# Kernel optimization log

Hardware: AMD Instinct MI355X
Metric: run time of the kernel (lower is better)

Reference implementation:

```python
import jax, jax.numpy as jnp
import numpy as np

B, S, H = 4, 1024, 2048
E = 16            # num_experts
K = 2             # num_experts_per_token
I = 1024          # per-expert intermediate_dim
N_SHARED = 2
I_SHARED = I * N_SHARED
RATIO = 0.1       # shared_expert_ratio
EPS = 1e-9


def _swiglu(x, wg, wu, wd):
    # SwiGLU, bias=False: down( silu(gate(x)) * up(x) )
    return (jax.nn.silu(x @ wg) * (x @ wu)) @ wd


def setup_inputs() -> dict:
    key = jax.random.key(0)
    ks = jax.random.split(key, 9)
    scale = 0.02
    x = jax.random.normal(ks[0], (B, S, H), dtype=jnp.float32)
    centroids = jax.random.normal(ks[1], (E, H), dtype=jnp.float32)  # nn.Parameter(randn)
    gate_bias = jnp.zeros((E,), dtype=jnp.float32)
    # shared expert SwiGLU weights (intermediate = I * n_shared_experts)
    wg_s = jax.random.normal(ks[2], (H, I_SHARED), dtype=jnp.float32) * scale
    wu_s = jax.random.normal(ks[3], (H, I_SHARED), dtype=jnp.float32) * scale
    wd_s = jax.random.normal(ks[4], (I_SHARED, H), dtype=jnp.float32) * scale
    # routed experts, stacked [E, ...]
    wg = jax.random.normal(ks[5], (E, H, I), dtype=jnp.float32) * scale
    wu = jax.random.normal(ks[6], (E, H, I), dtype=jnp.float32) * scale
    wd = jax.random.normal(ks[7], (E, I, H), dtype=jnp.float32) * scale
    return {"x": x, "centroids": centroids, "gate_bias": gate_bias,
            "wg_s": wg_s, "wu_s": wu_s, "wd_s": wd_s,
            "wg": wg, "wu": wu, "wd": wd}


def reference(x, centroids, gate_bias, wg_s, wu_s, wd_s, wg, wu, wd):
    # 1) shared expert on ALL tokens, scaled by ratio
    shared = _swiglu(x, wg_s, wu_s, wd_s) * RATIO          # [B,S,H]
    # 2) centroid affinity (DeepSeek-V3 sigmoid gating)
    affinity = jax.nn.sigmoid(jnp.einsum('bsh,eh->bse', x, centroids))  # [B,S,E]
    # 3) bias used ONLY for selection
    biased = affinity + gate_bias
    _, top_idx = jax.lax.top_k(biased, K)                  # [B,S,K]
    # 4) clean weights from unbiased affinity, normalized to sum 1
    top_aff = jnp.take_along_axis(affinity, top_idx, axis=-1)  # [B,S,K]
    weights = top_aff / (top_aff.sum(-1, keepdims=True) + EPS)
    # 5) combine-mask: per-token per-expert weight (0 if not selected)
    mask = (jax.nn.one_hot(top_idx, E, dtype=x.dtype) * weights[..., None]).sum(-2)  # [B,S,E]
    # 6) expert compute + weighted combine; loop over fixed small E avoids
    #    materializing a [B,S,E,H] tensor
    routed = jnp.zeros_like(x)
    for e in range(E):
        routed = routed + mask[..., e:e + 1] * _swiglu(x, wg[e], wu[e], wd[e])
    return shared + routed
```

## Files before the change

### kernel.cpp

```cpp
#include <hip/hip_runtime.h>
#include <hip/hip_bf16.h>

typedef unsigned short u16;
typedef unsigned int u32;
typedef unsigned long long u64;
typedef __attribute__((ext_vector_type(8))) short short8;
typedef __attribute__((ext_vector_type(4))) float f32x4;

#define TOKENS 4096
#define HDIM 2048
#define NEXP 16
#define IDIM 1024
#define ISH 2048
#define NCHUNK 128

#define GUITEMS 2304
#define DITEMS 2048

#define AS1(p) ((const __attribute__((address_space(1))) u32*)(p))
#define AS3(p) ((__attribute__((address_space(3))) u32*)(p))

__device__ __forceinline__ u16 f2b(float f) {
    u32 u = __float_as_uint(f);
    u32 r = u + 0x7fffu + ((u >> 16) & 1u);
    return (u16)(r >> 16);
}

__device__ __forceinline__ int item_index(int bid) {
    int x = bid & 7, j = bid >> 3;
    return ((x + 8 * (j >> 4)) << 4) | (j & 15);
}

__global__ __launch_bounds__(256) void route_kernel(const float* __restrict__ x,
                                                    const float* __restrict__ cent,
                                                    const float* __restrict__ bias,
                                                    u16* __restrict__ xb,
                                                    int* __restrict__ top_e,
                                                    float* __restrict__ top_w) {
    __shared__ alignas(16) float cs[8 * 2048];
    int lane = threadIdx.x & 63;
    int wv = threadIdx.x >> 6;
    int t = blockIdx.x * 4 + wv;
    const float4* xp4 = (const float4*)(x + (size_t)t * HDIM);
    float4 xr[8];
#pragma unroll
    for (int i = 0; i < 8; i++) xr[i] = xp4[lane + 64 * i];
    u16* xbp = xb + (size_t)t * HDIM;
#pragma unroll
    for (int i = 0; i < 8; i++) {
        u32 lo = (u32)f2b(xr[i].x) | ((u32)f2b(xr[i].y) << 16);
        u32 hi = (u32)f2b(xr[i].z) | ((u32)f2b(xr[i].w) << 16);
        uint2 o = make_uint2(lo, hi);
        *(uint2*)(xbp + (size_t)(lane + 64 * i) * 4) = o;
    }
    float aff[16];
#pragma unroll
    for (int ph = 0; ph < 2; ph++) {
        if (ph) __syncthreads();
        const float* sbase = cent + (size_t)(ph * 8 + wv * 2) * HDIM;
        float* dbase = cs + (size_t)wv * 2 * HDIM;
#pragma unroll
        for (int i = 0; i < 16; i++) {
            __builtin_amdgcn_global_load_lds(AS1(sbase + i * 256 + lane * 4),
                                             AS3(dbase + i * 256), 16, 0, 0);
        }
        __syncthreads();
#pragma unroll
        for (int e = 0; e < 8; e++) {
            const float4* cp = (const float4*)cs + (size_t)e * 512;
            float s = 0.f;
#pragma unroll
            for (int i = 0; i < 8; i++) {
                float4 cv = cp[lane + 64 * i];
                s += xr[i].x * cv.x;
                s += xr[i].y * cv.y;
                s += xr[i].z * cv.z;
                s += xr[i].w * cv.w;
            }
#pragma unroll
            for (int off = 32; off > 0; off >>= 1) s += __shfl_xor(s, off, 64);
            aff[ph * 8 + e] = 1.f / (1.f + expf(-s));
        }
    }
    float b0 = -1e30f, b1 = -1e30f, a0 = 0.f, a1 = 0.f;
    int e0 = -1, e1 = -1;
#pragma unroll
    for (int e = 0; e < 16; e++) {
        float v = aff[e] + bias[e];
        if (v > b0) {
            b1 = b0; e1 = e0; a1 = a0;
            b0 = v; e0 = e; a0 = aff[e];
        } else if (v > b1) {
            b1 = v; e1 = e; a1 = aff[e];
        }
    }
    float inv = 1.f / (a0 + a1 + 1e-9f);
    if (lane == 0) {
        top_e[2 * t] = e0; top_w[2 * t] = a0 * inv;
        top_e[2 * t + 1] = e1; top_w[2 * t + 1] = a1 * inv;
    }
}

__global__ __launch_bounds__(1024) void build_kernel(
    const int* __restrict__ top_e, const float* __restrict__ top_w,
    int* __restrict__ counts, int* __restrict__ offsets, int* __restrict__ itemsGU,
    int* __restrict__ itemsD, int* __restrict__ list_tok, int* __restrict__ tok2slot) {
    __shared__ int cnt[NCHUNK][16];
    __shared__ int offs_s[16];
    __shared__ int totals[16];
    __shared__ int guPref[16], dPref[16];
    int tid = threadIdx.x;
    int lane = tid & 63, wv = tid >> 6;
    for (int i = tid; i < GUITEMS; i += 1024) itemsGU[i] = -1;
    for (int i = tid; i < DITEMS; i += 1024) itemsD[i] = -1;
    for (int c = wv; c < NCHUNK; c += 16) {
        int v = top_e[c * 64 + lane];
#pragma unroll
        for (int e = 0; e < 16; e++) {
            u64 m = __ballot(v == e);
            if (lane == 0) cnt[c][e] = (int)__popcll(m);
        }
    }
    __syncthreads();
    if (tid < 16) {
        int s = 0;
        for (int c = 0; c < NCHUNK; c++) s += cnt[c][tid];
        totals[tid] = s;
        counts[tid] = s;
    }
    __syncthreads();
    if (tid == 0) {
        int r = 0, g = 0, d = 0;
        for (int e = 0; e < 16; e++) {
            offs_s[e] = r;
            offsets[e] = r;
            r += totals[e];
            guPref[e] = g;
            g += ((totals[e] + 127) >> 7) * 16;
            dPref[e] = d;
            d += ((totals[e] + 255) >> 8) * 32;
        }
    }
    {
        int i = tid;
        int g = i >> 4, s = i & 15;
        int y0 = (g >> 3) << 2, m0 = (g & 7) << 2;
        itemsGU[i] = ((m0 + (s >> 2)) << 8) | (y0 + (s & 3));
    }
    if (tid < 512) {
        int i = tid;
        int g = i >> 4, s = i & 15;
        int y0 = (g >> 2) << 2, m0 = (g & 3) << 2;
        itemsD[i] = ((m0 + (s >> 2)) << 8) | (y0 + (s & 3));
    }
    __syncthreads();
    if (tid < 16) {
        int e = tid;
        int tA = (totals[e] + 127) >> 7;
        int p = 1024 + guPref[e];
        for (int y0 = 0; y0 < 16; y0 += 4)
            for (int m = 0; m < tA; m++)
                for (int dy = 0; dy < 4; dy++)
                    itemsGU[p++] = (1 << 28) | (e << 20) | (m << 8) | (y0 + dy);
        int tB = (totals[e] + 255) >> 8;
        p = 512 + dPref[e];
        for (int y0 = 0; y0 < 32; y0 += 4)
            for (int m = 0; m < tB; m++)
                for (int dy = 0; dy < 4; dy++)
                    itemsD[p++] = (1 << 28) | (e << 20) | (m << 8) | (y0 + dy);
        int r = offs_s[e];
        for (int c = 0; c < NCHUNK; c++) {
            int v = cnt[c][e];
            cnt[c][e] = r;
            r += v;
        }
    }
    __syncthreads();
    for (int c = wv; c < NCHUNK; c += 16) {
        int i = c * 64 + lane;
        int v = top_e[i];
        int rank = 0;
#pragma unroll
        for (int e = 0; e < 16; e++) {
            u64 m = __ballot(v == e);
            if (v == e) rank = (int)__popcll(m & ((1ull << lane) - 1ull));
        }
        int slot = cnt[c][v] + rank;
        list_tok[slot] = i >> 1;
        tok2slot[i] = slot;
    }
}

__global__ __launch_bounds__(256) void conv_all_kernel(
    const float* __restrict__ wgs, const float* __restrict__ wus,
    const float* __restrict__ wds, const float* __restrict__ wg,
    const float* __restrict__ wu, const float* __restrict__ wd, u16* __restrict__ Wt_gs,
    u16* __restrict__ Wt_us, u16* __restrict__ Wt_ds, u16* __restrict__ Wt_g,
    u16* __restrict__ Wt_u, u16* __restrict__ Wt_d) {
    int id = blockIdx.x;
    const float* Wm;
    u16* Wtm;
    int K, N, nt, kc;
    if (id < 768) {
        K = 2048; N = 2048;
        int seg = id >> 8, r = id & 255;
        nt = r & 31; kc = r >> 5;
        if (seg == 0) { Wm = wgs; Wtm = Wt_gs; }
        else if (seg == 1) { Wm = wus; Wtm = Wt_us; }
        else { Wm = wds; Wtm = Wt_ds; }
    } else if (id < 4864) {
        K = 2048; N = 1024;
        int r = id - 768;
        int m = r >> 11;
        r &= 2047;
        int e = r >> 7;
        r &= 127;
        nt = r & 15; kc = r >> 4;
        size_t off = (size_t)e * 2048 * 1024;
        if (m == 0) { Wm = wg + off; Wtm = Wt_g + off; }
        else { Wm = wu + off; Wtm = Wt_u + off; }
    } else {
        K = 1024; N = 2048;
        int r = id - 4864;
        int e = r >> 7;
        r &= 127;
        nt = r & 31; kc = r >> 5;
        size_t off = (size_t)e * 1024 * 2048;
        Wm = wd + off; Wtm = Wt_d + off;
    }
    int ksB = K >> 5;
    __shared__ u16 Ls[64 * 40];
    int t = threadIdx.x;
    int kr = t >> 3, ng = t & 7;
    int nn = t >> 2, seg2 = t & 3;
    int g = seg2 ^ ((nn >> 2) & 3);
#pragma unroll
    for (int s = 0; s < 8; s++) {
        int kb = kc * 256 + s * 32;
        const float* src = Wm + (size_t)(kb + kr) * N + nt * 64 + ng * 8;
        float4 f0 = *(const float4*)src;
        float4 f1 = *(const float4*)(src + 4);
        __syncthreads();
        const float* p0 = (const float*)&f0;
        const float* p1 = (const float*)&f1;
#pragma unroll
        for (int l = 0; l < 4; l++) Ls[(8 * ng + l) * 40 + kr] = f2b(p0[l]);
#pragma unroll
        for (int l = 0; l < 4; l++) Ls[(8 * ng + 4 + l) * 40 + kr] = f2b(p1[l]);
        __syncthreads();
        const u16* lp = &Ls[nn * 40 + g * 8];
        u32 w0 = (u32)lp[0] | ((u32)lp[1] << 16);
        u32 w1 = (u32)lp[2] | ((u32)lp[3] << 16);
        u32 w2 = (u32)lp[4] | ((u32)lp[5] << 16);
        u32 w3 = (u32)lp[6] | ((u32)lp[7] << 16);
        uint4 o = make_uint4(w0, w1, w2, w3);
        *(uint4*)(Wtm + (size_t)(nt * ksB + (kb >> 5)) * 2048 + t * 8) = o;
    }
}

__global__ __launch_bounds__(256) void gemm_gateup(
    const u16* __restrict__ A, const u16* __restrict__ BgS, const u16* __restrict__ BuS,
    const u16* __restrict__ BgR, const u16* __restrict__ BuR, u16* __restrict__ hS,
    u16* __restrict__ hR, const int* __restrict__ counts, const int* __restrict__ offsets,
    const int* __restrict__ list_tok, const int* __restrict__ items) {
    int it = items[item_index(blockIdx.x)];
    if (it < 0) return;
    int routed = (it >> 28) & 1;
    int e = (it >> 20) & 15;
    int m0 = ((it >> 8) & 4095) * 128;
    int yb = it & 255;
    int cnt, base, Nout;
    const u16 *Bg, *Bu;
    u16* hout;
    if (routed) {
        cnt = counts[e];
        base = offsets[e];
        Nout = IDIM;
        size_t off = (size_t)e * HDIM * IDIM;
        Bg = BgR + off;
        Bu = BuR + off;
        hout = hR;
    } else {
        cnt = TOKENS;
        base = 0;
        Nout = ISH;
        Bg = BgS;
        Bu = BuS;
        hout = hS;
    }
    const int nk = HDIM >> 6;
    __shared__ alignas(16) u16 As[128 * 64];
    __shared__ alignas(16) u16 Bgs[64 * 64];
    __shared__ alignas(16) u16 Bus[64 * 64];
    int tid = threadIdx.x;
    int lane = tid & 63, wv = tid >> 6;
    int quad = lane >> 4, mr = lane & 15;
    int n0 = yb * 64;
    int gk = (tid & 3) ^ ((tid >> 4) & 3);
    int mg0 = min(m0 + (tid >> 2), cnt - 1);
    int mg1 = min(m0 + 64 + (tid >> 2), cnt - 1);
    size_t sr0 = routed ? (size_t)list_tok[base + mg0] : (size_t)mg0;
    size_t sr1 = routed ? (size_t)list_tok[base + mg1] : (size_t)mg1;
    const u16* ap0 = A + sr0 * HDIM + gk * 8;
    const u16* ap1 = A + sr1 * HDIM + gk * 8;
    size_t bstr = (size_t)(HDIM >> 5) * 2048;
    const u16* bgp = Bg + (size_t)yb * bstr + tid * 8;
    const u16* bup = Bu + (size_t)yb * bstr + tid * 8;
    int xq = quad ^ ((mr >> 2) & 3);
    f32x4 accg[2][4], accu[2][4];
#pragma unroll
    for (int i = 0; i < 2; i++)
#pragma unroll
        for (int j = 0; j < 4; j++) { accg[i][j] = (f32x4)0.f; accu[i][j] = (f32x4)0.f; }

    for (int ks = 0; ks < nk; ks++) {
        __syncthreads();
        __builtin_amdgcn_global_load_lds(AS1(ap0), AS3(As + wv * 512), 16, 0, 0);
        __builtin_amdgcn_global_load_lds(AS1(ap0 + 32), AS3(As + 4096 + wv * 512), 16, 0, 0);
        __builtin_amdgcn_global_load_lds(AS1(ap1), AS3(As + 2048 + wv * 512), 16, 0, 0);
        __builtin_amdgcn_global_load_lds(AS1(ap1 + 32), AS3(As + 6144 + wv * 512), 16, 0, 0);
        __builtin_amdgcn_global_load_lds(AS1(bgp), AS3(Bgs + wv * 512), 16, 0, 0);
        __builtin_amdgcn_global_load_lds(AS1(bgp + 2048), AS3(Bgs + 2048 + wv * 512), 16, 0, 0);
        __builtin_amdgcn_global_load_lds(AS1(bup), AS3(Bus + wv * 512), 16, 0, 0);
        __builtin_amdgcn_global_load_lds(AS1(bup + 2048), AS3(Bus + 2048 + wv * 512), 16, 0, 0);
        ap0 += 64; ap1 += 64; bgp += 4096; bup += 4096;
        __syncthreads();
#pragma unroll
        for (int c = 0; c < 2; c++) {
            short8 a0 = *(const short8*)(As + c * 4096 + ((32 * wv + mr) * 4 + xq) * 8);
            short8 a1 = *(const short8*)(As + c * 4096 + ((32 * wv + 16 + mr) * 4 + xq) * 8);
#pragma unroll
            for (int j = 0; j < 4; j++) {
                short8 bg = *(const short8*)(Bgs + c * 2048 + (64 * j + mr * 4 + xq) * 8);
                short8 bu = *(const short8*)(Bus + c * 2048 + (64 * j + mr * 4 + xq) * 8);
                accg[0][j] = __builtin_amdgcn_mfma_f32_16x16x32_bf16(a0, bg, accg[0][j], 0, 0, 0);
                accg[1][j] = __builtin_amdgcn_mfma_f32_16x16x32_bf16(a1, bg, accg[1][j], 0, 0, 0);
                accu[0][j] = __builtin_amdgcn_mfma_f32_16x16x32_bf16(a0, bu, accu[0][j], 0, 0, 0);
                accu[1][j] = __builtin_amdgcn_mfma_f32_16x16x32_bf16(a1, bu, accu[1][j], 0, 0, 0);
            }
        }
    }
#pragma unroll
    for (int i = 0; i < 2; i++)
#pragma unroll
        for (int j = 0; j < 4; j++)
#pragma unroll
            for (int r = 0; r < 4; r++) {
                int m = m0 + 32 * wv + 16 * i + quad * 4 + r;
                if (m < cnt) {
                    float gv = accg[i][j][r], uv = accu[i][j][r];
                    float h = gv / (1.f + expf(-gv)) * uv;
                    int n = n0 + 16 * j + mr;
                    hout[(size_t)(base + m) * Nout + n] = f2b(h);
                }
            }
}

__global__ __launch_bounds__(256) void gemm_down(
    const u16* __restrict__ hS, const u16* __restrict__ hR, const u16* __restrict__ BdS,
    const u16* __restrict__ BdR, float* __restrict__ out, float* __restrict__ rd,
    const int* __restrict__ counts, const int* __restrict__ offsets,
    const int* __restrict__ items) {
    int it = items[item_index(blockIdx.x)];
    if (it < 0) return;
    int routed = (it >> 28) & 1;
    int e = (it >> 20) & 15;
    int m0 = ((it >> 8) & 4095) * 256;
    int yb = it & 255;
    int cnt, base, Kd;
    const u16 *A, *B;
    float* outp;
    if (routed) {
        cnt = counts[e];
        base = offsets[e];
        Kd = IDIM;
        A = hR;
        B = BdR + (size_t)e * IDIM * HDIM;
        outp = rd;
    } else {
        cnt = TOKENS;
        base = 0;
        Kd = ISH;
        A = hS;
        B = BdS;
        outp = out;
    }
    int nk = Kd >> 6;
    __shared__ alignas(16) u16 As[256 * 64];
    __shared__ alignas(16) u16 Bs[64 * 64];
    int tid = threadIdx.x;
    int lane = tid & 63, wv = tid >> 6;
    int quad = lane >> 4, mr = lane & 15;
    int n0 = yb * 64;
    int gk = (tid & 3) ^ ((tid >> 4) & 3);
    const u16* ap0;
    const u16* ap1;
    const u16* ap2;
    const u16* ap3;
    {
        int mg0 = base + min(m0 + 0 * 64 + (tid >> 2), cnt - 1);
        int mg1 = base + min(m0 + 1 * 64 + (tid >> 2), cnt - 1);
        int mg2 = base + min(m0 + 2 * 64 + (tid >> 2), cnt - 1);
        int mg3 = base + min(m0 + 3 * 64 + (tid >> 2), cnt - 1);
        ap0 = A + (size_t)mg0 * Kd + gk * 8;
        ap1 = A + (size_t)mg1 * Kd + gk * 8;
        ap2 = A + (size_t)mg2 * Kd + gk * 8;
        ap3 = A + (size_t)mg3 * Kd + gk * 8;
    }
    size_t bstr = (size_t)(Kd >> 5) * 2048;
    const u16* bp = B + (size_t)yb * bstr + tid * 8;
    int xq = quad ^ ((mr >> 2) & 3);
    f32x4 acc[4][4];
#pragma unroll
    for (int i = 0; i < 4; i++)
#pragma unroll
        for (int j = 0; j < 4; j++) acc[i][j] = (f32x4)0.f;

    for (int ks = 0; ks < nk; ks++) {
        __syncthreads();
        __builtin_amdgcn_global_load_lds(AS1(ap0), AS3(As + 0 + wv * 512), 16, 0, 0);
        __builtin_amdgcn_global_load_lds(AS1(ap0 + 32), AS3(As + 8192 + wv * 512), 16, 0, 0);
        __builtin_amdgcn_global_load_lds(AS1(ap1), AS3(As + 2048 + wv * 512), 16, 0, 0);
        __builtin_amdgcn_global_load_lds(AS1(ap1 + 32), AS3(As + 10240 + wv * 512), 16, 0, 0);
        __builtin_amdgcn_global_load_lds(AS1(ap2), AS3(As + 4096 + wv * 512), 16, 0, 0);
        __builtin_amdgcn_global_load_lds(AS1(ap2 + 32), AS3(As + 12288 + wv * 512), 16, 0, 0);
        __builtin_amdgcn_global_load_lds(AS1(ap3), AS3(As + 6144 + wv * 512), 16, 0, 0);
        __builtin_amdgcn_global_load_lds(AS1(ap3 + 32), AS3(As + 14336 + wv * 512), 16, 0, 0);
        __builtin_amdgcn_global_load_lds(AS1(bp), AS3(Bs + wv * 512), 16, 0, 0);
        __builtin_amdgcn_global_load_lds(AS1(bp + 2048), AS3(Bs + 2048 + wv * 512), 16, 0, 0);
        ap0 += 64; ap1 += 64; ap2 += 64; ap3 += 64; bp += 4096;
        __syncthreads();
#pragma unroll
        for (int c = 0; c < 2; c++) {
            short8 a0 = *(const short8*)(As + c * 8192 + ((64 * wv + 0 + mr) * 4 + xq) * 8);
            short8 a1 = *(const short8*)(As + c * 8192 + ((64 * wv + 16 + mr) * 4 + xq) * 8);
            short8 a2 = *(const short8*)(As + c * 8192 + ((64 * wv + 32 + mr) * 4 + xq) * 8);
            short8 a3 = *(const short8*)(As + c * 8192 + ((64 * wv + 48 + mr) * 4 + xq) * 8);
#pragma unroll
            for (int j = 0; j < 4; j++) {
                short8 b = *(const short8*)(Bs + c * 2048 + (64 * j + mr * 4 + xq) * 8);
                acc[0][j] = __builtin_amdgcn_mfma_f32_16x16x32_bf16(a0, b, acc[0][j], 0, 0, 0);
                acc[1][j] = __builtin_amdgcn_mfma_f32_16x16x32_bf16(a1, b, acc[1][j], 0, 0, 0);
                acc[2][j] = __builtin_amdgcn_mfma_f32_16x16x32_bf16(a2, b, acc[2][j], 0, 0, 0);
                acc[3][j] = __builtin_amdgcn_mfma_f32_16x16x32_bf16(a3, b, acc[3][j], 0, 0, 0);
            }
        }
    }

#pragma unroll
    for (int i = 0; i < 4; i++)
#pragma unroll
        for (int j = 0; j < 4; j++)
#pragma unroll
            for (int r = 0; r < 4; r++) {
                int m = m0 + 64 * wv + 16 * i + quad * 4 + r;
                if (m >= cnt) continue;
                int n = n0 + 16 * j + mr;
                float v = acc[i][j][r];
                if (routed) {
                    outp[(size_t)(base + m) * HDIM + n] = v;
                } else {
                    outp[(size_t)m * HDIM + n] = 0.1f * v;
                }
            }
}

__global__ __launch_bounds__(256) void combine_kernel(float* __restrict__ out,
                                                      const float* __restrict__ rd,
                                                      const int* __restrict__ tok2slot,
                                                      const float* __restrict__ top_w) {
    int t = blockIdx.x;
    int s0 = tok2slot[2 * t], s1 = tok2slot[2 * t + 1];
    float w0 = top_w[2 * t], w1 = top_w[2 * t + 1];
    const float4* r0 = (const float4*)(rd + (size_t)s0 * HDIM);
    const float4* r1 = (const float4*)(rd + (size_t)s1 * HDIM);
    float4* op = (float4*)(out + (size_t)t * HDIM);
#pragma unroll
    for (int k = 0; k < 2; k++) {
        int c = threadIdx.x + k * 256;
        float4 o = op[c];
        float4 a = r0[c];
        float4 b = r1[c];
        o.x += w0 * a.x + w1 * b.x;
        o.y += w0 * a.y + w1 * b.y;
        o.z += w0 * a.z + w1 * b.z;
        o.w += w0 * a.w + w1 * b.w;
        op[c] = o;
    }
}

extern "C" void kernel_launch(void* const* d_in, const int* in_sizes, int n_in,
                              void* d_out, int out_size, void* d_ws, size_t ws_size,
                              hipStream_t stream) {
    const float* x = (const float*)d_in[0];
    const float* cent = (const float*)d_in[1];
    const float* bias = (const float*)d_in[2];
    const float* wgs = (const float*)d_in[3];
    const float* wus = (const float*)d_in[4];
    const float* wds = (const float*)d_in[5];
    const float* wg = (const float*)d_in[6];
    const float* wu = (const float*)d_in[7];
    const float* wd = (const float*)d_in[8];
    float* out = (float*)d_out;
    char* ws = (char*)d_ws;

    size_t off_wtgs = 0;
    size_t off_wtus = off_wtgs + (size_t)HDIM * ISH * 2;
    size_t off_wtds = off_wtus + (size_t)HDIM * ISH * 2;
    size_t off_wtg = off_wtds + (size_t)ISH * HDIM * 2;
    size_t off_wtu = off_wtg + (size_t)NEXP * HDIM * IDIM * 2;
    size_t off_wtd = off_wtu + (size_t)NEXP * HDIM * IDIM * 2;
    size_t off_xbf = off_wtd + (size_t)NEXP * IDIM * HDIM * 2;
    size_t off_hsh = off_xbf + (size_t)TOKENS * HDIM * 2;
    size_t off_hrt = off_hsh + (size_t)TOKENS * ISH * 2;
    size_t off_meta = off_hrt + (size_t)2 * TOKENS * IDIM * 2;
    size_t need = off_meta + (1 << 20);
    if (ws_size < need) return;

    u16* Wt_gs = (u16*)(ws + off_wtgs);
    u16* Wt_us = (u16*)(ws + off_wtus);
    u16* Wt_ds = (u16*)(ws + off_wtds);
    u16* Wt_g = (u16*)(ws + off_wtg);
    u16* Wt_u = (u16*)(ws + off_wtu);
    u16* Wt_d = (u16*)(ws + off_wtd);
    u16* x_bf = (u16*)(ws + off_xbf);
    u16* h_sh = (u16*)(ws + off_hsh);
    u16* h_rt = (u16*)(ws + off_hrt);
    float* rd = (float*)(ws + off_wtg);
    int* counts = (int*)(ws + off_meta);
    int* offsets = counts + 16;
    int* itemsGU = offsets + 16;
    int* itemsD = itemsGU + GUITEMS;
    int* tok2slot = itemsD + DITEMS;
    int* top_e = tok2slot + 2 * TOKENS;
    float* top_w = (float*)(top_e + 2 * TOKENS);
    int* list_tok = (int*)(top_w + 2 * TOKENS);

    route_kernel<<<TOKENS / 4, 256, 0, stream>>>(x, cent, bias, x_bf, top_e, top_w);
    build_kernel<<<1, 1024, 0, stream>>>(top_e, top_w, counts, offsets, itemsGU, itemsD,
                                         list_tok, tok2slot);
    conv_all_kernel<<<6912, 256, 0, stream>>>(wgs, wus, wds, wg, wu, wd, Wt_gs, Wt_us,
                                              Wt_ds, Wt_g, Wt_u, Wt_d);
    gemm_gateup<<<GUITEMS, 256, 0, stream>>>(x_bf, Wt_gs, Wt_us, Wt_g, Wt_u, h_sh, h_rt,
                                             counts, offsets, list_tok, itemsGU);
    gemm_down<<<DITEMS, 256, 0, stream>>>(h_sh, h_rt, Wt_ds, Wt_d, out, rd, counts,
                                          offsets, itemsD);
    combine_kernel<<<TOKENS, 256, 0, stream>>>(out, rd, tok2slot, top_w);
}
```

Baseline: 865.8 us.

## Split gate and up GEMMs across separate warp groups in gate-up kernel

The gate-up kernel now launches 512 threads, with four waves computing the gate projection and four computing the up projection. This halves the per-wave accumulators to allow higher occupancy (launch bounds 512,4). The up results pass through a new 32 KB LDS buffer so the gate waves can apply SiLU and the product. This raises shared memory per block and adds an extra barrier plus an LDS round trip in the epilogue.

Result: no change. 859.1 us (-0.8%).

```diff
diff --git a/kernel.cpp b/kernel.cpp
--- a/kernel.cpp
+++ b/kernel.cpp
@@ -258,7 +258,7 @@
     }
 }
 
-__global__ __launch_bounds__(256) void gemm_gateup(
+__global__ __launch_bounds__(512, 4) void gemm_gateup(
     const u16* __restrict__ A, const u16* __restrict__ BgS, const u16* __restrict__ BuS,
     const u16* __restrict__ BgR, const u16* __restrict__ BuR, u16* __restrict__ hS,
     u16* __restrict__ hR, const int* __restrict__ counts, const int* __restrict__ offsets,
@@ -292,68 +292,79 @@
     __shared__ alignas(16) u16 As[128 * 64];
     __shared__ alignas(16) u16 Bgs[64 * 64];
     __shared__ alignas(16) u16 Bus[64 * 64];
+    __shared__ alignas(16) float us[128 * 64];
     int tid = threadIdx.x;
     int lane = tid & 63, wv = tid >> 6;
+    int wl = wv & 3, mat = wv >> 2;
     int quad = lane >> 4, mr = lane & 15;
     int n0 = yb * 64;
     int gk = (tid & 3) ^ ((tid >> 4) & 3);
     int mg0 = min(m0 + (tid >> 2), cnt - 1);
-    int mg1 = min(m0 + 64 + (tid >> 2), cnt - 1);
     size_t sr0 = routed ? (size_t)list_tok[base + mg0] : (size_t)mg0;
-    size_t sr1 = routed ? (size_t)list_tok[base + mg1] : (size_t)mg1;
     const u16* ap0 = A + sr0 * HDIM + gk * 8;
-    const u16* ap1 = A + sr1 * HDIM + gk * 8;
     size_t bstr = (size_t)(HDIM >> 5) * 2048;
-    const u16* bgp = Bg + (size_t)yb * bstr + tid * 8;
-    const u16* bup = Bu + (size_t)yb * bstr + tid * 8;
+    const u16* bsrc = (mat ? Bu : Bg) + (size_t)yb * bstr + (size_t)(tid & 255) * 8;
+    u16* bdstW = (mat ? Bus : Bgs) + wl * 512;
+    u16* adstW = As + wv * 512;
+    const u16* bbuf = mat ? Bus : Bgs;
     int xq = quad ^ ((mr >> 2) & 3);
-    f32x4 accg[2][4], accu[2][4];
+    f32x4 acc[2][4];
 #pragma unroll
     for (int i = 0; i < 2; i++)
 #pragma unroll
-        for (int j = 0; j < 4; j++) { accg[i][j] = (f32x4)0.f; accu[i][j] = (f32x4)0.f; }
+        for (int j = 0; j < 4; j++) acc[i][j] = (f32x4)0.f;
 
     for (int ks = 0; ks < nk; ks++) {
         __syncthreads();
-        __builtin_amdgcn_global_load_lds(AS1(ap0), AS3(As + wv * 512), 16, 0, 0);
-        __builtin_amdgcn_global_load_lds(AS1(ap0 + 32), AS3(As + 4096 + wv * 512), 16, 0, 0);
-        __builtin_amdgcn_global_load_lds(AS1(ap1), AS3(As + 2048 + wv * 512), 16, 0, 0);
-        __builtin_amdgcn_global_load_lds(AS1(ap1 + 32), AS3(As + 6144 + wv * 512), 16, 0, 0);
-        __builtin_amdgcn_global_load_lds(AS1(bgp), AS3(Bgs + wv * 512), 16, 0, 0);
-        __builtin_amdgcn_global_load_lds(AS1(bgp + 2048), AS3(Bgs + 2048 + wv * 512), 16, 0, 0);
-        __builtin_amdgcn_global_load_lds(AS1(bup), AS3(Bus + wv * 512), 16, 0, 0);
-        __builtin_amdgcn_global_load_lds(AS1(bup + 2048), AS3(Bus + 2048 + wv * 512), 16, 0, 0);
-        ap0 += 64; ap1 += 64; bgp += 4096; bup += 4096;
+        __builtin_amdgcn_global_load_lds(AS1(ap0), AS3(adstW), 16, 0, 0);
+        __builtin_amdgcn_global_load_lds(AS1(ap0 + 32), AS3(adstW + 4096), 16, 0, 0);
+        __builtin_amdgcn_global_load_lds(AS1(bsrc), AS3(bdstW), 16, 0, 0);
+        __builtin_amdgcn_global_load_lds(AS1(bsrc + 2048), AS3(bdstW + 2048), 16, 0, 0);
+        ap0 += 64; bsrc += 4096;
         __syncthreads();
 #pragma unroll
         for (int c = 0; c < 2; c++) {
-            short8 a0 = *(const short8*)(As + c * 4096 + ((32 * wv + mr) * 4 + xq) * 8);
-            short8 a1 = *(const short8*)(As + c * 4096 + ((32 * wv + 16 + mr) * 4 + xq) * 8);
+            short8 a0 = *(const short8*)(As + c * 4096 + ((32 * wl + mr) * 4 + xq) * 8);
+            short8 a1 = *(const short8*)(As + c * 4096 + ((32 * wl + 16 + mr) * 4 + xq) * 8);
 #pragma unroll
             for (int j = 0; j < 4; j++) {
-                short8 bg = *(const short8*)(Bgs + c * 2048 + (64 * j + mr * 4 + xq) * 8);
-                short8 bu = *(const short8*)(Bus + c * 2048 + (64 * j + mr * 4 + xq) * 8);
-                accg[0][j] = __builtin_amdgcn_mfma_f32_16x16x32_bf16(a0, bg, accg[0][j], 0, 0, 0);
-                accg[1][j] = __builtin_amdgcn_mfma_f32_16x16x32_bf16(a1, bg, accg[1][j], 0, 0, 0);
-                accu[0][j] = __builtin_amdgcn_mfma_f32_16x16x32_bf16(a0, bu, accu[0][j], 0, 0, 0);
-                accu[1][j] = __builtin_amdgcn_mfma_f32_16x16x32_bf16(a1, bu, accu[1][j], 0, 0, 0);
+                short8 b = *(const short8*)(bbuf + c * 2048 + (64 * j + mr * 4 + xq) * 8);
+                acc[0][j] = __builtin_amdgcn_mfma_f32_16x16x32_bf16(a0, b, acc[0][j], 0, 0, 0);
+                acc[1][j] = __builtin_amdgcn_mfma_f32_16x16x32_bf16(a1, b, acc[1][j], 0, 0, 0);
             }
         }
     }
-#pragma unroll
-    for (int i = 0; i < 2; i++)
-#pragma unroll
-        for (int j = 0; j < 4; j++)
-#pragma unroll
-            for (int r = 0; r < 4; r++) {
-                int m = m0 + 32 * wv + 16 * i + quad * 4 + r;
-                if (m < cnt) {
-                    float gv = accg[i][j][r], uv = accu[i][j][r];
-                    float h = gv / (1.f + expf(-gv)) * uv;
-                    int n = n0 + 16 * j + mr;
-                    hout[(size_t)(base + m) * Nout + n] = f2b(h);
+    __syncthreads();
+    if (mat == 1) {
+#pragma unroll
+        for (int i = 0; i < 2; i++)
+#pragma unroll
+            for (int j = 0; j < 4; j++)
+#pragma unroll
+                for (int r = 0; r < 4; r++) {
+                    int row = 32 * wl + 16 * i + quad * 4 + r;
+                    us[row * 64 + 16 * j + mr] = acc[i][j][r];
                 }
-            }
+    }
+    __syncthreads();
+    if (mat == 0) {
+#pragma unroll
+        for (int i = 0; i < 2; i++)
+#pragma unroll
+            for (int j = 0; j < 4; j++)
+#pragma unroll
+                for (int r = 0; r < 4; r++) {
+                    int row = 32 * wl + 16 * i + quad * 4 + r;
+                    int m = m0 + row;
+                    if (m < cnt) {
+                        float gv = acc[i][j][r];
+                        float uv = us[row * 64 + 16 * j + mr];
+                        float h = gv / (1.f + expf(-gv)) * uv;
+                        int n = n0 + 16 * j + mr;
+                        hout[(size_t)(base + m) * Nout + n] = f2b(h);
+                    }
+                }
+    }
 }
 
 __global__ __launch_bounds__(256) void gemm_down(
@@ -541,7 +552,7 @@
                                          list_tok, tok2slot);
     conv_all_kernel<<<6912, 256, 0, stream>>>(wgs, wus, wds, wg, wu, wd, Wt_gs, Wt_us,
                                               Wt_ds, Wt_g, Wt_u, Wt_d);
-    gemm_gateup<<<GUITEMS, 256, 0, stream>>>(x_bf, Wt_gs, Wt_us, Wt_g, Wt_u, h_sh, h_rt,
+    gemm_gateup<<<GUITEMS, 512, 0, stream>>>(x_bf, Wt_gs, Wt_us, Wt_g, Wt_u, h_sh, h_rt,
                                              counts, offsets, list_tok, itemsGU);
     gemm_down<<<DITEMS, 256, 0, stream>>>(h_sh, h_rt, Wt_ds, Wt_d, out, rd, counts,
                                           offsets, itemsD);
```
